# Kernel optimization log

Hardware: AMD Instinct MI355X
Metric: run time of the kernel (lower is better)

The kernel has to match this reference:

```python
import jax, jax.numpy as jnp
import numpy as np


def setup_inputs() -> dict:
    key = jax.random.key(0)
    k1, k2, k3, k4, k5 = jax.random.split(key, 5)
    B, T, U, D, H, V = 4, 256, 64, 512, 512, 1024
    return {
        "encoder_outputs": jax.random.normal(k1, (B, T, D), dtype=jnp.float32),
        "decoder_outputs": jax.random.normal(k2, (B, U, D), dtype=jnp.float32),
        "W1": jax.random.normal(k3, (2 * D, H), dtype=jnp.float32) * 0.02,
        "b1": jax.random.normal(k4, (H,), dtype=jnp.float32) * 0.02,
        "W2": jax.random.normal(k5, (H, V), dtype=jnp.float32) * 0.02,
    }


def reference(encoder_outputs, decoder_outputs, W1, b1, W2):
    # Original torch code materializes concat([enc_tile, dec_tile], -1) of shape
    # [B, T, U, 2D] then applies Linear(2D->H) -> tanh -> Linear(H->V, no bias).
    # Mathematically identical: split W1 into encoder/decoder halves, project each
    # sequence once, and broadcast-add over (T, U).
    D = encoder_outputs.shape[-1]
    W1_enc, W1_dec = W1[:D], W1[D:]
    enc_proj = jnp.einsum("btd,dh->bth", encoder_outputs, W1_enc)  # [B,T,H]
    dec_proj = jnp.einsum("bud,dh->buh", decoder_outputs, W1_dec)  # [B,U,H]
    hidden = jnp.tanh(enc_proj[:, :, None, :] + dec_proj[:, None, :, :] + b1)  # [B,T,U,H]
    return jnp.einsum("btuh,hv->btuv", hidden, W2)  # [B,T,U,V]
```

## Files before the change

kernel.cpp:

```cpp
#include <hip/hip_runtime.h>
#include <hip/hip_bf16.h>
#include <stdint.h>

typedef __attribute__((ext_vector_type(4))) float f32x4;
typedef __attribute__((ext_vector_type(4))) unsigned int u32x4;
typedef __attribute__((ext_vector_type(8))) short bf16x8;

static __device__ __forceinline__ unsigned short f2bf(float f) {
  union { float f; unsigned int u; } v; v.f = f;
  unsigned int r = v.u + 0x7fffu + ((v.u >> 16) & 1u);
  return (unsigned short)(r >> 16);
}
static __device__ __forceinline__ unsigned int pack2(float lo, float hi) {
  return ((unsigned int)f2bf(hi) << 16) | (unsigned int)f2bf(lo);
}
static __device__ __forceinline__ float tanh_fast(float x) {
  x = fminf(9.0f, fmaxf(-9.0f, x));
  float t = __builtin_amdgcn_exp2f(x * 2.885390081777927f);
  return (t - 1.0f) * __builtin_amdgcn_rcpf(t + 1.0f);
}
static __device__ __forceinline__ bf16x8 as_bf16x8(u32x4 v) {
  union { u32x4 u; bf16x8 b; } c; c.u = v; return c.b;
}

#define GLOAD_LDS16(gp, lp)                                                   \
  __builtin_amdgcn_global_load_lds(                                           \
      (const __attribute__((address_space(1))) unsigned int*)(gp),            \
      (__attribute__((address_space(3))) unsigned int*)(lp), 16, 0, 0)

__global__ void transpose_cvt_kernel(const float* __restrict__ src,
                                     unsigned short* __restrict__ dst,
                                     int R, int C) {
  __shared__ float tile[32][33];
  const int c0 = blockIdx.x * 32, r0 = blockIdx.y * 32;
  const int tx = threadIdx.x, ty = threadIdx.y;
#pragma unroll
  for (int i = 0; i < 4; ++i)
    tile[ty + i * 8][tx] = src[(size_t)(r0 + ty + i * 8) * C + c0 + tx];
  __syncthreads();
#pragma unroll
  for (int i = 0; i < 4; ++i)
    dst[(size_t)(c0 + ty + i * 8) * R + r0 + tx] = f2bf(tile[tx][ty + i * 8]);
}

__global__ __launch_bounds__(256) void proj_kernel(
    const float* __restrict__ enc, const float* __restrict__ dec,
    const unsigned short* __restrict__ W1T, const float* __restrict__ b1,
    float* __restrict__ projBuf) {
  __shared__ u32x4 lsA[64 * 8];
  __shared__ u32x4 lsB[64 * 8];
  const int tid = threadIdx.x;
  const int lane = tid & 63, wid = tid >> 6;
  const int wr = wid >> 1, wc = wid & 1;
  const int m0 = blockIdx.x * 64, n0 = blockIdx.y * 64;
  const int koff = (m0 >= 1024) ? 512 : 0;
  const int l15 = lane & 15, l4 = lane >> 4;
  const int rrB = lane >> 3;
  const int sblkB = (lane & 7) ^ rrB;

  f32x4 acc[2][2] = {};

  for (int kt = 0; kt < 8; ++kt) {
    const int k0 = kt * 64;
    if (kt) __syncthreads();
#pragma unroll
    for (int i = 0; i < 2; ++i) {
      const int rbase = wid * 16 + i * 8;
      const unsigned short* g =
          W1T + (size_t)(n0 + rbase + rrB) * 1024 + koff + k0 + sblkB * 8;
      GLOAD_LDS16(g, &lsB[rbase * 8]);
    }
    {
      const int r = tid >> 2;
      const int kk = (tid & 3) << 4;
      const int m = m0 + r;
      const float* g = (m < 1024) ? (enc + (size_t)m * 512 + k0 + kk)
                                  : (dec + (size_t)(m - 1024) * 512 + k0 + kk);
      u32x4 w0, w1;
      f32x4 v;
      v = *(const f32x4*)(g + 0);  w0[0] = pack2(v[0], v[1]); w0[1] = pack2(v[2], v[3]);
      v = *(const f32x4*)(g + 4);  w0[2] = pack2(v[0], v[1]); w0[3] = pack2(v[2], v[3]);
      v = *(const f32x4*)(g + 8);  w1[0] = pack2(v[0], v[1]); w1[1] = pack2(v[2], v[3]);
      v = *(const f32x4*)(g + 12); w1[2] = pack2(v[0], v[1]); w1[3] = pack2(v[2], v[3]);
      const int b0 = kk >> 3, rs = r & 7;
      lsA[r * 8 + (b0 ^ rs)] = w0;
      lsA[r * 8 + ((b0 + 1) ^ rs)] = w1;
    }
    __syncthreads();
#pragma unroll
    for (int kf = 0; kf < 2; ++kf) {
      bf16x8 a[2], b[2];
#pragma unroll
      for (int mf = 0; mf < 2; ++mf) {
        const int row = wr * 32 + mf * 16 + l15;
        a[mf] = as_bf16x8(lsA[row * 8 + (((kf << 2) + l4) ^ (row & 7))]);
      }
#pragma unroll
      for (int nf = 0; nf < 2; ++nf) {
        const int row = wc * 32 + nf * 16 + l15;
        b[nf] = as_bf16x8(lsB[row * 8 + (((kf << 2) + l4) ^ (row & 7))]);
      }
#pragma unroll
      for (int mf = 0; mf < 2; ++mf)
#pragma unroll
        for (int nf = 0; nf < 2; ++nf)
          acc[mf][nf] = __builtin_amdgcn_mfma_f32_16x16x32_bf16(
              a[mf], b[nf], acc[mf][nf], 0, 0, 0);
    }
  }
#pragma unroll
  for (int mf = 0; mf < 2; ++mf) {
    const int row0 = m0 + wr * 32 + mf * 16 + l4 * 4;
#pragma unroll
    for (int nf = 0; nf < 2; ++nf) {
      const int col = n0 + wc * 32 + nf * 16 + l15;
      const float bias = (m0 >= 1024) ? b1[col] : 0.0f;
#pragma unroll
      for (int j = 0; j < 4; ++j)
        projBuf[(size_t)(row0 + j) * 512 + col] = acc[mf][nf][j] + bias;
    }
  }
}

__global__ __launch_bounds__(512, 2) void joint_kernel(
    const float* __restrict__ projBuf, const unsigned short* __restrict__ W2T,
    float* __restrict__ out) {
  __shared__ u32x4 lsA[128 * 8];
  __shared__ u32x4 lsB[256 * 8];
  const int tid = threadIdx.x;
  const int lane = tid & 63, wid = tid >> 6;
  const int wr = wid >> 2, wc = wid & 3;
  const int m0 = blockIdx.x * 128;
  const int n0 = blockIdx.y * 256;
  const int e0 = m0 >> 6;
  const int dbase = 1024 + ((m0 >> 14) << 6);
  const int l15 = lane & 15, l4 = lane >> 4;

  f32x4 acc[4][4] = {};

  const int r = tid >> 2;
  const int kk = (tid & 3) << 4;
  const float* geBase = projBuf + ((size_t)(e0 + (r >> 6)) << 9) + kk;
  const float* gdBase = projBuf + ((size_t)(dbase + (r & 63)) << 9) + kk;
  const int b0 = kk >> 3, rs = r & 7;
  const int rrB = lane >> 3;
  const int sblkB = (lane & 7) ^ rrB;

  for (int kt = 0; kt < 8; ++kt) {
    const int k0 = kt * 64;
    if (kt) __syncthreads();
#pragma unroll
    for (int i = 0; i < 4; ++i) {
      const int rbase = wid * 32 + i * 8;
      const unsigned short* g =
          W2T + (size_t)(n0 + rbase + rrB) * 512 + k0 + sblkB * 8;
      GLOAD_LDS16(g, &lsB[rbase * 8]);
    }
    {
      const float* ge = geBase + k0;
      const float* gd = gdBase + k0;
      u32x4 w0, w1;
      f32x4 e, d;
      e = *(const f32x4*)(ge + 0);  d = *(const f32x4*)(gd + 0);
      w0[0] = pack2(tanh_fast(e[0] + d[0]), tanh_fast(e[1] + d[1]));
      w0[1] = pack2(tanh_fast(e[2] + d[2]), tanh_fast(e[3] + d[3]));
      e = *(const f32x4*)(ge + 4);  d = *(const f32x4*)(gd + 4);
      w0[2] = pack2(tanh_fast(e[0] + d[0]), tanh_fast(e[1] + d[1]));
      w0[3] = pack2(tanh_fast(e[2] + d[2]), tanh_fast(e[3] + d[3]));
      e = *(const f32x4*)(ge + 8);  d = *(const f32x4*)(gd + 8);
      w1[0] = pack2(tanh_fast(e[0] + d[0]), tanh_fast(e[1] + d[1]));
      w1[1] = pack2(tanh_fast(e[2] + d[2]), tanh_fast(e[3] + d[3]));
      e = *(const f32x4*)(ge + 12); d = *(const f32x4*)(gd + 12);
      w1[2] = pack2(tanh_fast(e[0] + d[0]), tanh_fast(e[1] + d[1]));
      w1[3] = pack2(tanh_fast(e[2] + d[2]), tanh_fast(e[3] + d[3]));
      lsA[r * 8 + (b0 ^ rs)] = w0;
      lsA[r * 8 + ((b0 + 1) ^ rs)] = w1;
    }
    __syncthreads();
#pragma unroll
    for (int kf = 0; kf < 2; ++kf) {
      bf16x8 a[4], b[4];
#pragma unroll
      for (int mf = 0; mf < 4; ++mf) {
        const int row = wr * 64 + mf * 16 + l15;
        a[mf] = as_bf16x8(lsA[row * 8 + (((kf << 2) + l4) ^ (l15 & 7))]);
      }
#pragma unroll
      for (int nf = 0; nf < 4; ++nf) {
        const int row = wc * 64 + nf * 16 + l15;
        b[nf] = as_bf16x8(lsB[row * 8 + (((kf << 2) + l4) ^ (l15 & 7))]);
      }
#pragma unroll
      for (int mf = 0; mf < 4; ++mf)
#pragma unroll
        for (int nf = 0; nf < 4; ++nf)
          acc[mf][nf] = __builtin_amdgcn_mfma_f32_16x16x32_bf16(
              a[mf], b[nf], acc[mf][nf], 0, 0, 0);
    }
  }
#pragma unroll
  for (int mf = 0; mf < 4; ++mf) {
    const size_t row0 = (size_t)(m0 + wr * 64 + mf * 16 + l4 * 4);
#pragma unroll
    for (int nf = 0; nf < 4; ++nf) {
      const int col = n0 + wc * 64 + nf * 16 + l15;
#pragma unroll
      for (int j = 0; j < 4; ++j)
        out[(row0 + j) * 1024 + col] = acc[mf][nf][j];
    }
  }
}

extern "C" void kernel_launch(void* const* d_in, const int* in_sizes, int n_in,
                              void* d_out, int out_size, void* d_ws, size_t ws_size,
                              hipStream_t stream) {
  const float* enc = (const float*)d_in[0];
  const float* dec = (const float*)d_in[1];
  const float* W1  = (const float*)d_in[2];
  const float* b1  = (const float*)d_in[3];
  const float* W2  = (const float*)d_in[4];
  float* out = (float*)d_out;

  char* ws = (char*)d_ws;
  unsigned short* W1T = (unsigned short*)ws;
  unsigned short* W2T = (unsigned short*)(ws + (1 << 20));
  float* projBuf = (float*)(ws + (2 << 20));

  transpose_cvt_kernel<<<dim3(512 / 32, 1024 / 32), dim3(32, 8), 0, stream>>>(
      W1, W1T, 1024, 512);
  transpose_cvt_kernel<<<dim3(1024 / 32, 512 / 32), dim3(32, 8), 0, stream>>>(
      W2, W2T, 512, 1024);
  proj_kernel<<<dim3(20, 8), 256, 0, stream>>>(enc, dec, W1T, b1, projBuf);
  joint_kernel<<<dim3(512, 4), 512, 0, stream>>>(projBuf, W2T, out);
}
```

Baseline: 424.5 us.

## Materialize bf16 tanh hidden tensor, then run plain bf16 GEMM with swizzled tiles

Result: faster. 382.6 us (-9.9%).

```diff
diff --git a/kernel.cpp b/kernel.cpp
--- a/kernel.cpp
+++ b/kernel.cpp
@@ -118,6 +118,97 @@
 #pragma unroll
       for (int j = 0; j < 4; ++j)
         projBuf[(size_t)(row0 + j) * 512 + col] = acc[mf][nf][j] + bias;
+    }
+  }
+}
+
+__global__ __launch_bounds__(256) void hidden_kernel(
+    const float* __restrict__ projBuf, unsigned short* __restrict__ hid) {
+  const int tid = threadIdx.x;
+  const int m = blockIdx.x * 8 + (tid >> 5);
+  const int h0 = (tid & 31) * 16;
+  const float* ge = projBuf + ((size_t)(m >> 6) << 9) + h0;
+  const float* gd =
+      projBuf + ((size_t)(1024 + ((m >> 14) << 6) + (m & 63)) << 9) + h0;
+  u32x4 w0, w1;
+  f32x4 e, d;
+  e = *(const f32x4*)(ge + 0);  d = *(const f32x4*)(gd + 0);
+  w0[0] = pack2(tanh_fast(e[0] + d[0]), tanh_fast(e[1] + d[1]));
+  w0[1] = pack2(tanh_fast(e[2] + d[2]), tanh_fast(e[3] + d[3]));
+  e = *(const f32x4*)(ge + 4);  d = *(const f32x4*)(gd + 4);
+  w0[2] = pack2(tanh_fast(e[0] + d[0]), tanh_fast(e[1] + d[1]));
+  w0[3] = pack2(tanh_fast(e[2] + d[2]), tanh_fast(e[3] + d[3]));
+  e = *(const f32x4*)(ge + 8);  d = *(const f32x4*)(gd + 8);
+  w1[0] = pack2(tanh_fast(e[0] + d[0]), tanh_fast(e[1] + d[1]));
+  w1[1] = pack2(tanh_fast(e[2] + d[2]), tanh_fast(e[3] + d[3]));
+  e = *(const f32x4*)(ge + 12); d = *(const f32x4*)(gd + 12);
+  w1[2] = pack2(tanh_fast(e[0] + d[0]), tanh_fast(e[1] + d[1]));
+  w1[3] = pack2(tanh_fast(e[2] + d[2]), tanh_fast(e[3] + d[3]));
+  unsigned short* o = hid + ((size_t)m << 9) + h0;
+  *(u32x4*)(o) = w0;
+  *(u32x4*)(o + 8) = w1;
+}
+
+__global__ __launch_bounds__(256) void gemm_kernel(
+    const unsigned short* __restrict__ hid,
+    const unsigned short* __restrict__ W2T, float* __restrict__ out) {
+  __shared__ u32x4 lsA[128 * 8];
+  __shared__ u32x4 lsB[128 * 8];
+  const int tid = threadIdx.x;
+  const int lane = tid & 63, wid = tid >> 6;
+  const int wr = wid >> 1, wc = wid & 1;
+  const int bid = blockIdx.x;
+  const int sid = (bid & 7) * 512 + (bid >> 3);
+  const int m0 = (sid >> 3) * 128;
+  const int n0 = (sid & 7) * 128;
+  const int l15 = lane & 15, l4 = lane >> 4;
+  const int rr = lane >> 3;
+  const int sblk = (lane & 7) ^ rr;
+
+  f32x4 acc[4][4] = {};
+  const unsigned short* gA = hid + (size_t)(m0 + rr) * 512 + sblk * 8;
+  const unsigned short* gB = W2T + (size_t)(n0 + rr) * 512 + sblk * 8;
+
+  for (int kt = 0; kt < 8; ++kt) {
+    const int k0 = kt * 64;
+    if (kt) __syncthreads();
+#pragma unroll
+    for (int i = 0; i < 4; ++i) {
+      const int rbase = wid * 32 + i * 8;
+      GLOAD_LDS16(gA + (size_t)rbase * 512 + k0, &lsA[rbase * 8]);
+      GLOAD_LDS16(gB + (size_t)rbase * 512 + k0, &lsB[rbase * 8]);
+    }
+    __syncthreads();
+#pragma unroll
+    for (int kf = 0; kf < 2; ++kf) {
+      bf16x8 a[4], b[4];
+#pragma unroll
+      for (int mf = 0; mf < 4; ++mf) {
+        const int row = wr * 64 + mf * 16 + l15;
+        a[mf] = as_bf16x8(lsA[row * 8 + (((kf << 2) + l4) ^ (row & 7))]);
+      }
+#pragma unroll
+      for (int nf = 0; nf < 4; ++nf) {
+        const int row = wc * 64 + nf * 16 + l15;
+        b[nf] = as_bf16x8(lsB[row * 8 + (((kf << 2) + l4) ^ (row & 7))]);
+      }
+#pragma unroll
+      for (int mf = 0; mf < 4; ++mf)
+#pragma unroll
+        for (int nf = 0; nf < 4; ++nf)
+          acc[mf][nf] = __builtin_amdgcn_mfma_f32_16x16x32_bf16(
+              a[mf], b[nf], acc[mf][nf], 0, 0, 0);
+    }
+  }
+#pragma unroll
+  for (int mf = 0; mf < 4; ++mf) {
+    const size_t row0 = (size_t)(m0 + wr * 64 + mf * 16 + l4 * 4);
+#pragma unroll
+    for (int nf = 0; nf < 4; ++nf) {
+      const int col = n0 + wc * 64 + nf * 16 + l15;
+#pragma unroll
+      for (int j = 0; j < 4; ++j)
+        out[(row0 + j) * 1024 + col] = acc[mf][nf][j];
     }
   }
 }
@@ -225,11 +316,17 @@
   unsigned short* W1T = (unsigned short*)ws;
   unsigned short* W2T = (unsigned short*)(ws + (1 << 20));
   float* projBuf = (float*)(ws + (2 << 20));
-
-  transpose_cvt_kernel<<<dim3(512 / 32, 1024 / 32), dim3(32, 8), 0, stream>>>(
-      W1, W1T, 1024, 512);
-  transpose_cvt_kernel<<<dim3(1024 / 32, 512 / 32), dim3(32, 8), 0, stream>>>(
-      W2, W2T, 512, 1024);
+  unsigned short* hid = (unsigned short*)(ws + (5u << 20));
+  const size_t need = (5u << 20) + (64u << 20);
+
+  transpose_cvt_kernel<<<dim3(16, 32), dim3(32, 8), 0, stream>>>(W1, W1T, 1024, 512);
+  transpose_cvt_kernel<<<dim3(32, 16), dim3(32, 8), 0, stream>>>(W2, W2T, 512, 1024);
   proj_kernel<<<dim3(20, 8), 256, 0, stream>>>(enc, dec, W1T, b1, projBuf);
-  joint_kernel<<<dim3(512, 4), 512, 0, stream>>>(projBuf, W2T, out);
-}
+
+  if (ws_size >= need) {
+    hidden_kernel<<<8192, 256, 0, stream>>>(projBuf, hid);
+    gemm_kernel<<<4096, 256, 0, stream>>>(hid, W2T, out);
+  } else {
+    joint_kernel<<<dim3(512, 4), 512, 0, stream>>>(projBuf, W2T, out);
+  }
+}
```
